# Performance work log

Measured on AMD Instinct MI355X. Metric: run time of the kernel, lower is better.

Reference implementation:

```python
import jax, jax.numpy as jnp
import numpy as np

BETA = 0.35

def setup_inputs() -> dict:
    key = jax.random.key(0)
    k1, k2, k3 = jax.random.split(key, 3)
    B, D, C, O = 16384, 512, 4096, 128
    x = jax.random.normal(k1, (B, D), dtype=jnp.float32)
    centers = jax.random.normal(k2, (C, D), dtype=jnp.float32)
    W = jax.random.normal(k3, (C, O), dtype=jnp.float32) * (1.0 / np.sqrt(C))
    b = jnp.zeros((O,), dtype=jnp.float32)
    return {"x": x, "centers": centers, "W": W, "b": b}

def reference(x, centers, W, b):
    # Squared Euclidean distances via the GEMM identity ||a-b||^2 = ||a||^2 + ||b||^2 - 2 a.b
    # (same math as expand_dims/subtract/square/reduce_sum, avoids [B,C,D] intermediate)
    x_sq = jnp.sum(x * x, axis=1, keepdims=True)          # [B,1]
    c_sq = jnp.sum(centers * centers, axis=1)             # [C]
    cross = x @ centers.T                                  # [B,C]
    sq_dist = x_sq + c_sq[None, :] - 2.0 * cross           # [B,C]
    rbf = jnp.exp(-BETA * sq_dist)                         # [B,C]
    return rbf @ W + b                                      # [B,O]
```

## Files before the change

kernel.cpp:

```cpp
#include <hip/hip_runtime.h>
#include <hip/hip_bf16.h>

typedef short bf16x8 __attribute__((ext_vector_type(8)));
typedef float f32x4 __attribute__((ext_vector_type(4)));
typedef float f32x16 __attribute__((ext_vector_type(16)));
typedef long l64x2 __attribute__((ext_vector_type(2)));
typedef int i32x8 __attribute__((ext_vector_type(8)));
typedef unsigned short u16;
typedef unsigned char u8;

#define NB2 (-0.35f * 1.44269504088896340736f)
#define P2C (0.70f * 1.44269504088896340736f)
#define MFS(a,b,c) __builtin_amdgcn_mfma_scale_f32_32x32x64_f8f6f4( \
    a, b, c, 0, 0, 0, 0x7F7F7F7F, 0, 0x7F7F7F7F)
#define MFB(a,b,c) __builtin_amdgcn_mfma_f32_32x32x16_bf16(a, b, c, 0, 0, 0)

__device__ __forceinline__ u16 f2bf(float f) {
  union { float f; unsigned int u; } v; v.f = f;
  unsigned int x = v.u;
  return (u16)((x + 0x7FFFu + ((x >> 16) & 1u)) >> 16);
}

__device__ __forceinline__ unsigned cvtpk(float lo, float hi) {
  unsigned r;
  asm("v_cvt_pk_bf16_f32 %0, %1, %2" : "=v"(r) : "v"(lo), "v"(hi));
  return r;
}

__device__ __forceinline__ void pswap(unsigned &a, unsigned &b) {
  asm volatile("v_permlane32_swap_b32 %0, %1" : "+v"(a), "+v"(b));
}

__device__ __forceinline__ u8 f2e4m3(float f) {
  unsigned int u = __float_as_uint(f);
  u8 s = (u8)((u >> 24) & 0x80u);
  float a = fabsf(f);
  if (a >= 448.f) return s | 0x7E;
  if (a < 0.015625f) return s | (u8)(int)rintf(a * 512.f);
  unsigned int m = u & 0x7fffffffu;
  unsigned int r = m + 0x7FFFFu + ((m >> 20) & 1u);
  return s | (u8)((((r >> 23) - 120u) << 3) | ((r >> 20) & 7u));
}

__device__ __forceinline__ unsigned int pk4(float a, float b, float c, float d) {
#if __has_builtin(__builtin_amdgcn_cvt_pk_fp8_f32)
  int v = __builtin_amdgcn_cvt_pk_fp8_f32(a, b, 0, false);
  v = __builtin_amdgcn_cvt_pk_fp8_f32(c, d, v, true);
  return (unsigned int)v;
#else
  return (unsigned int)f2e4m3(a) | ((unsigned int)f2e4m3(b) << 8)
       | ((unsigned int)f2e4m3(c) << 16) | ((unsigned int)f2e4m3(d) << 24);
#endif
}

#define GLOAD_LDS(g, l) __builtin_amdgcn_global_load_lds( \
    (const __attribute__((address_space(1))) unsigned int*)(g), \
    (__attribute__((address_space(3))) unsigned int*)(l), 16, 0, 0)

__global__ __launch_bounds__(512)
void prep_x8(const float* __restrict__ src, u8* __restrict__ dst,
             float* __restrict__ sq) {
  const int row = blockIdx.x * 8 + (threadIdx.x >> 6);
  const int i6 = threadIdx.x & 63;
  const float4* p = (const float4*)(src + (size_t)row * 512) + i6 * 2;
  float4 a = p[0], b = p[1];
  float ss = a.x*a.x + a.y*a.y + a.z*a.z + a.w*a.w
           + b.x*b.x + b.y*b.y + b.z*b.z + b.w*b.w;
  uint2 o;
  o.x = pk4(a.x, a.y, a.z, a.w);
  o.y = pk4(b.x, b.y, b.z, b.w);
  const int P = i6 >> 3, rem = i6 & 7;
  const int kh = rem >> 2;
  const int l = (kh << 5) | (row & 31);
  *(uint2*)(dst + (size_t)(row >> 5) * 16384 + P * 2048 + l * 32 + (rem & 3) * 8) = o;
  ss += __shfl_xor(ss, 1);  ss += __shfl_xor(ss, 2);
  ss += __shfl_xor(ss, 4);  ss += __shfl_xor(ss, 8);
  ss += __shfl_xor(ss, 16); ss += __shfl_xor(ss, 32);
  if (i6 == 0) sq[row] = ss;
}

__global__ __launch_bounds__(256)
void prep_cen(const float* __restrict__ cen, u8* __restrict__ cfr,
              float* __restrict__ csq) {
  const int t = threadIdx.x;
  const int c = blockIdx.x * 4 + (t >> 6);
  const int i6 = t & 63;
  const float* p = cen + (size_t)c * 512 + i6 * 8;
  float4 a = *(const float4*)p, b = *(const float4*)(p + 4);
  float ss = a.x*a.x + a.y*a.y + a.z*a.z + a.w*a.w
           + b.x*b.x + b.y*b.y + b.z*b.z + b.w*b.w;
  uint2 o;
  o.x = pk4(a.x, a.y, a.z, a.w);
  o.y = pk4(b.x, b.y, b.z, b.w);
  const int P = i6 >> 3, rem = i6 & 7;
  const int kh = rem >> 2;
  const int lc = c & 31;
  const int l = (kh << 5) | lc;
  const int u = (rem >> 1) & 1;
  const int sub = rem & 1;
  const int us = u ^ ((lc >> 2) & 1);
  *(uint2*)(cfr + (size_t)(c >> 5) * 16384 + P * 2048 + l * 32 + us * 16 + sub * 8) = o;
  ss += __shfl_xor(ss, 1);  ss += __shfl_xor(ss, 2);
  ss += __shfl_xor(ss, 4);  ss += __shfl_xor(ss, 8);
  ss += __shfl_xor(ss, 16); ss += __shfl_xor(ss, 32);
  if (i6 == 0) csq[c] = ss;
}

__global__ __launch_bounds__(256)
void prep_w(const float* __restrict__ W, u8* __restrict__ wt) {
  __shared__ u16 t_[128 * 66];
  const int c0 = blockIdx.x * 64;
  const int t = threadIdx.x;
#pragma unroll
  for (int it = 0; it < 32; ++it) {
    int idx = it * 256 + t;
    int cl = idx >> 7;
    int o  = idx & 127;
    t_[o * 66 + cl] = f2bf(W[(size_t)(c0 + cl) * 128 + o]);
  }
  __syncthreads();
#pragma unroll
  for (int it = 0; it < 4; ++it) {
    int idx = it * 256 + t;
    int o  = idx >> 3;
    int uu = idx & 7;
    int ch = uu >> 2;
    int kt = (uu >> 1) & 1;
    int h2 = uu & 1;
    int u  = (kt * 2 + h2) ^ ((o >> 1) & 3);
    u16* d = (u16*)(wt + ((size_t)(c0 >> 5) + ch) * 8192 + o * 64 + u * 16);
    const u16* s_ = &t_[o * 66 + ch * 32 + kt * 16 + h2 * 8];
#pragma unroll
    for (int j = 0; j < 8; ++j) d[j] = s_[j];
  }
}

__global__ __launch_bounds__(256)
void init_out(const float* __restrict__ bias, float* __restrict__ out) {
  const int i4 = blockIdx.x * 256 + threadIdx.x;
  float4 b = ((const float4*)bias)[i4 & 31];
  ((float4*)out)[i4] = b;
}

__global__ __launch_bounds__(256, 2)
void rbf_main(const u8* __restrict__ xfs, const u8* __restrict__ cfr,
              const u8* __restrict__ wtgb, const float* __restrict__ csq_g,
              const float* __restrict__ xsq_g, float* __restrict__ out)
{
  __shared__ __align__(16) u8 cs[2][16384];
  __shared__ __align__(16) u8 wt[2][8192];
  __shared__ __align__(16) float csq_l[1024];
  __shared__ __align__(16) float xsq_l[128];

  const int tid = threadIdx.x;
  const int lane = tid & 63;
  const int wv = tid >> 6;
  const int l31 = lane & 31;
  const int h = lane >> 5;
  const int bid = blockIdx.x;
  const int chq = bid & 3;
  const size_t r0 = (size_t)(bid >> 2) * 128;

#define S_CS(cc) do { \
    const u8* sG_ = cfr + ((size_t)(chq * 32 + (cc)) << 14) + tid * 16; \
    u8* sL_ = &cs[(cc) & 1][0] + tid * 16; \
    GLOAD_LDS(sG_,         sL_); \
    GLOAD_LDS(sG_ + 4096,  sL_ + 4096); \
    GLOAD_LDS(sG_ + 8192,  sL_ + 8192); \
    GLOAD_LDS(sG_ + 12288, sL_ + 12288); \
  } while (0)

#define S_W(cc) do { \
    const u8* wg_ = wtgb + ((size_t)(chq * 32 + (cc)) << 13) + tid * 16; \
    u8* wl_ = &wt[(cc) & 1][0] + tid * 16; \
    GLOAD_LDS(wg_,        wl_); \
    GLOAD_LDS(wg_ + 4096, wl_ + 4096); \
  } while (0)

  if (tid < 32) GLOAD_LDS(xsq_g + r0 + tid * 4, xsq_l + tid * 4);
  GLOAD_LDS(csq_g + chq * 1024 + tid * 4, csq_l + tid * 4);
  S_CS(0);
  S_W(0);

  i32x8 xf8[8];
  {
    const u8* xb = xfs + ((size_t)((bid >> 2) * 4 + wv)) * 16384 + lane * 32;
#pragma unroll
    for (int P = 0; P < 8; ++P) {
      union { l64x2 q[2]; i32x8 v; } t;
      t.q[0] = *(const l64x2*)(xb + P * 2048);
      t.q[1] = *(const l64x2*)(xb + P * 2048 + 16);
      xf8[P] = t.v;
    }
  }

  asm volatile("s_waitcnt vmcnt(0)" ::: "memory");
  __builtin_amdgcn_s_barrier();
  __builtin_amdgcn_sched_barrier(0);

  const float xn = NB2 * xsq_l[wv * 32 + l31];

  const int swz = (lane >> 2) & 1;
  const int alo = lane * 32 + swz * 16;
  const int ahi = lane * 32 + (swz ^ 1) * 16;
  const int wsw = (l31 >> 1) & 3;
  const int wb_o = l31 * 64;
  const int wu0 = ((0 + h) ^ wsw) << 4;
  const int wu1 = ((2 + h) ^ wsw) << 4;

  const f32x16 z16 = {0,0,0,0,0,0,0,0,0,0,0,0,0,0,0,0};
  f32x16 oa0 = z16, oa1 = z16, oa2 = z16, oa3 = z16;

#pragma unroll 1
  for (int cc = 0; cc < 32; ++cc) {
    if (cc < 31) { S_CS(cc + 1); S_W(cc + 1); }
    const u8* csb = &cs[cc & 1][0];

    f32x16 s0 = z16, s1 = z16;
#pragma unroll
    for (int P = 0; P < 8; ++P) {
      union { l64x2 q[2]; i32x8 v; } A;
      A.q[0] = *(const l64x2*)(csb + P * 2048 + alo);
      A.q[1] = *(const l64x2*)(csb + P * 2048 + ahi);
      __builtin_amdgcn_s_setprio(1);
      if (P & 1) s1 = MFS(A.v, xf8[P], s1);
      else       s0 = MFS(A.v, xf8[P], s0);
      __builtin_amdgcn_s_setprio(0);
    }

    f32x4 cq0 = *(const f32x4*)(csq_l + cc * 32 + 0  + 4 * h);
    f32x4 cq1 = *(const f32x4*)(csq_l + cc * 32 + 8  + 4 * h);
    f32x4 cq2 = *(const f32x4*)(csq_l + cc * 32 + 16 + 4 * h);
    f32x4 cq3 = *(const f32x4*)(csq_l + cc * 32 + 24 + 4 * h);
    float e[16];
#pragma unroll
    for (int r = 0; r < 16; ++r) {
      const float cq = (r < 4 ? cq0[r] : r < 8 ? cq1[r - 4] : r < 12 ? cq2[r - 8] : cq3[r - 12]);
      e[r] = __builtin_amdgcn_exp2f(fmaf(s0[r] + s1[r], P2C, fmaf(cq, NB2, xn)));
    }
    unsigned P0 = cvtpk(e[0],  e[1]),  P1 = cvtpk(e[2],  e[3]);
    unsigned P2 = cvtpk(e[4],  e[5]),  P3 = cvtpk(e[6],  e[7]);
    unsigned P4 = cvtpk(e[8],  e[9]),  P5 = cvtpk(e[10], e[11]);
    unsigned P6 = cvtpk(e[12], e[13]), P7 = cvtpk(e[14], e[15]);
    pswap(P0, P2); pswap(P1, P3);
    pswap(P4, P6); pswap(P5, P7);
    union { unsigned u[4]; bf16x8 v; } FA, GA;
    FA.u[0] = P0; FA.u[1] = P1; FA.u[2] = P2; FA.u[3] = P3;
    GA.u[0] = P4; GA.u[1] = P5; GA.u[2] = P6; GA.u[3] = P7;

    {
      const u8* wtb = &wt[cc & 1][0];
      bf16x8 wA0 = *(const bf16x8*)(wtb + wb_o + wu0);
      bf16x8 wB0 = *(const bf16x8*)(wtb + wb_o + wu1);
      bf16x8 wA1 = *(const bf16x8*)(wtb + 2048 + wb_o + wu0);
      bf16x8 wB1 = *(const bf16x8*)(wtb + 2048 + wb_o + wu1);
      __builtin_amdgcn_s_setprio(1);
      oa0 = MFB(FA.v, wA0, oa0);
      oa0 = MFB(GA.v, wB0, oa0);
      oa1 = MFB(FA.v, wA1, oa1);
      oa1 = MFB(GA.v, wB1, oa1);
      __builtin_amdgcn_s_setprio(0);
      bf16x8 wA2 = *(const bf16x8*)(wtb + 4096 + wb_o + wu0);
      bf16x8 wB2 = *(const bf16x8*)(wtb + 4096 + wb_o + wu1);
      bf16x8 wA3 = *(const bf16x8*)(wtb + 6144 + wb_o + wu0);
      bf16x8 wB3 = *(const bf16x8*)(wtb + 6144 + wb_o + wu1);
      __builtin_amdgcn_s_setprio(1);
      oa2 = MFB(FA.v, wA2, oa2);
      oa2 = MFB(GA.v, wB2, oa2);
      oa3 = MFB(FA.v, wA3, oa3);
      oa3 = MFB(GA.v, wB3, oa3);
      __builtin_amdgcn_s_setprio(0);
    }

    asm volatile("s_waitcnt vmcnt(0)" ::: "memory");
    __builtin_amdgcn_s_barrier();
    __builtin_amdgcn_sched_barrier(0);
  }

#pragma unroll
  for (int r = 0; r < 16; ++r) {
    const int m = wv * 32 + (r & 3) + 8 * (r >> 2) + 4 * h;
    float* op = &out[(r0 + m) * 128 + l31];
    atomicAdd(op,      oa0[r]);
    atomicAdd(op + 32, oa1[r]);
    atomicAdd(op + 64, oa2[r]);
    atomicAdd(op + 96, oa3[r]);
  }
#undef S_CS
#undef S_W
}

extern "C" void kernel_launch(void* const* d_in, const int* in_sizes, int n_in,
                              void* d_out, int out_size, void* d_ws, size_t ws_size,
                              hipStream_t stream) {
  (void)in_sizes; (void)n_in; (void)out_size; (void)ws_size;
  const float* x   = (const float*)d_in[0];
  const float* cen = (const float*)d_in[1];
  const float* W   = (const float*)d_in[2];
  const float* b   = (const float*)d_in[3];
  u8* xfs = (u8*)d_ws;
  u8* cfr = xfs + (size_t)16384 * 512;
  u8* wtgb = cfr + (size_t)4096 * 512;
  float* csq = (float*)(wtgb + (size_t)128 * 4096 * 2);
  float* xsq = csq + 4096;
  prep_x8<<<2048, 512, 0, stream>>>(x, xfs, xsq);
  prep_cen<<<1024, 256, 0, stream>>>(cen, cfr, csq);
  prep_w<<<64, 256, 0, stream>>>(W, wtgb);
  init_out<<<2048, 256, 0, stream>>>(b, (float*)d_out);
  rbf_main<<<512, 256, 0, stream>>>(xfs, cfr, wtgb, csq, xsq, (float*)d_out);
}
```

Measured before the change: 93.51 us.

## Switch second GEMM to FP8 scaled MFMA with W fragments read from global

Replaces the bf16 rbf@W stage with FP8 e4m3 scaled MFMA (32x32x64). W is pre-quantized with a 64x scale compensated by the MFMA scale exponent, and the rbf values are packed to fp8. Each iteration now processes two center chunks (K=64), and W fragments are loaded directly from global into registers instead of being staged in LDS. The center tile buffer grows to four slots so two chunks are prefetched per step. This halves the MFMA count and W bandwidth for the second GEMM and removes the W LDS traffic, at the cost of lower precision in the rbf and W operands.

```diff
diff --git a/kernel.cpp b/kernel.cpp
--- a/kernel.cpp
+++ b/kernel.cpp
@@ -1,7 +1,6 @@
 #include <hip/hip_runtime.h>
 #include <hip/hip_bf16.h>
 
-typedef short bf16x8 __attribute__((ext_vector_type(8)));
 typedef float f32x4 __attribute__((ext_vector_type(4)));
 typedef float f32x16 __attribute__((ext_vector_type(16)));
 typedef long l64x2 __attribute__((ext_vector_type(2)));
@@ -13,19 +12,8 @@
 #define P2C (0.70f * 1.44269504088896340736f)
 #define MFS(a,b,c) __builtin_amdgcn_mfma_scale_f32_32x32x64_f8f6f4( \
     a, b, c, 0, 0, 0, 0x7F7F7F7F, 0, 0x7F7F7F7F)
-#define MFB(a,b,c) __builtin_amdgcn_mfma_f32_32x32x16_bf16(a, b, c, 0, 0, 0)
-
-__device__ __forceinline__ u16 f2bf(float f) {
-  union { float f; unsigned int u; } v; v.f = f;
-  unsigned int x = v.u;
-  return (u16)((x + 0x7FFFu + ((x >> 16) & 1u)) >> 16);
-}
-
-__device__ __forceinline__ unsigned cvtpk(float lo, float hi) {
-  unsigned r;
-  asm("v_cvt_pk_bf16_f32 %0, %1, %2" : "=v"(r) : "v"(lo), "v"(hi));
-  return r;
-}
+#define MFS2(a,b,c) __builtin_amdgcn_mfma_scale_f32_32x32x64_f8f6f4( \
+    a, b, c, 0, 0, 0, 0x7F7F7F7F, 0, 0x79797979)
 
 __device__ __forceinline__ void pswap(unsigned &a, unsigned &b) {
   asm volatile("v_permlane32_swap_b32 %0, %1" : "+v"(a), "+v"(b));
@@ -107,32 +95,25 @@
 }
 
 __global__ __launch_bounds__(256)
-void prep_w(const float* __restrict__ W, u8* __restrict__ wt) {
-  __shared__ u16 t_[128 * 66];
-  const int c0 = blockIdx.x * 64;
+void prep_w(const float* __restrict__ W, u8* __restrict__ wfr) {
+  __shared__ float t_[64 * 128];
+  const int pr = blockIdx.x;
   const int t = threadIdx.x;
 #pragma unroll
   for (int it = 0; it < 32; ++it) {
     int idx = it * 256 + t;
-    int cl = idx >> 7;
-    int o  = idx & 127;
-    t_[o * 66 + cl] = f2bf(W[(size_t)(c0 + cl) * 128 + o]);
+    t_[idx] = W[(size_t)(pr * 64 + (idx >> 7)) * 128 + (idx & 127)];
   }
   __syncthreads();
-#pragma unroll
-  for (int it = 0; it < 4; ++it) {
-    int idx = it * 256 + t;
-    int o  = idx >> 3;
-    int uu = idx & 7;
-    int ch = uu >> 2;
-    int kt = (uu >> 1) & 1;
-    int h2 = uu & 1;
-    int u  = (kt * 2 + h2) ^ ((o >> 1) & 3);
-    u16* d = (u16*)(wt + ((size_t)(c0 >> 5) + ch) * 8192 + o * 64 + u * 16);
-    const u16* s_ = &t_[o * 66 + ch * 32 + kt * 16 + h2 * 8];
-#pragma unroll
-    for (int j = 0; j < 8; ++j) d[j] = s_[j];
-  }
+  const int l = t & 63, ot = t >> 6;
+  const int kh = l >> 5, o = ot * 32 + (l & 31);
+  u8 buf[32];
+#pragma unroll
+  for (int b = 0; b < 32; ++b)
+    buf[b] = f2e4m3(64.f * t_[(kh * 32 + b) * 128 + o]);
+  u8* d = wfr + (size_t)pr * 8192 + ot * 2048 + l * 32;
+  *(uint4*)d = *(uint4*)buf;
+  *(uint4*)(d + 16) = *(uint4*)(buf + 16);
 }
 
 __global__ __launch_bounds__(256)
@@ -144,11 +125,10 @@
 
 __global__ __launch_bounds__(256, 2)
 void rbf_main(const u8* __restrict__ xfs, const u8* __restrict__ cfr,
-              const u8* __restrict__ wtgb, const float* __restrict__ csq_g,
+              const u8* __restrict__ wfr, const float* __restrict__ csq_g,
               const float* __restrict__ xsq_g, float* __restrict__ out)
 {
-  __shared__ __align__(16) u8 cs[2][16384];
-  __shared__ __align__(16) u8 wt[2][8192];
+  __shared__ __align__(16) u8 cs[4][16384];
   __shared__ __align__(16) float csq_l[1024];
   __shared__ __align__(16) float xsq_l[128];
 
@@ -163,24 +143,17 @@
 
 #define S_CS(cc) do { \
     const u8* sG_ = cfr + ((size_t)(chq * 32 + (cc)) << 14) + tid * 16; \
-    u8* sL_ = &cs[(cc) & 1][0] + tid * 16; \
+    u8* sL_ = &cs[(cc) & 3][0] + tid * 16; \
     GLOAD_LDS(sG_,         sL_); \
     GLOAD_LDS(sG_ + 4096,  sL_ + 4096); \
     GLOAD_LDS(sG_ + 8192,  sL_ + 8192); \
     GLOAD_LDS(sG_ + 12288, sL_ + 12288); \
   } while (0)
 
-#define S_W(cc) do { \
-    const u8* wg_ = wtgb + ((size_t)(chq * 32 + (cc)) << 13) + tid * 16; \
-    u8* wl_ = &wt[(cc) & 1][0] + tid * 16; \
-    GLOAD_LDS(wg_,        wl_); \
-    GLOAD_LDS(wg_ + 4096, wl_ + 4096); \
-  } while (0)
-
   if (tid < 32) GLOAD_LDS(xsq_g + r0 + tid * 4, xsq_l + tid * 4);
   GLOAD_LDS(csq_g + chq * 1024 + tid * 4, csq_l + tid * 4);
   S_CS(0);
-  S_W(0);
+  S_CS(1);
 
   i32x8 xf8[8];
   {
@@ -203,74 +176,66 @@
   const int swz = (lane >> 2) & 1;
   const int alo = lane * 32 + swz * 16;
   const int ahi = lane * 32 + (swz ^ 1) * 16;
-  const int wsw = (l31 >> 1) & 3;
-  const int wb_o = l31 * 64;
-  const int wu0 = ((0 + h) ^ wsw) << 4;
-  const int wu1 = ((2 + h) ^ wsw) << 4;
 
   const f32x16 z16 = {0,0,0,0,0,0,0,0,0,0,0,0,0,0,0,0};
   f32x16 oa0 = z16, oa1 = z16, oa2 = z16, oa3 = z16;
 
+#define G1EXP(CC, SLOT, O0, O1, O2, O3) do { \
+    const u8* csb = &cs[SLOT][0]; \
+    f32x16 s0 = z16, s1 = z16; \
+    _Pragma("unroll") \
+    for (int P = 0; P < 8; ++P) { \
+      union { l64x2 q[2]; i32x8 v; } A; \
+      A.q[0] = *(const l64x2*)(csb + P * 2048 + alo); \
+      A.q[1] = *(const l64x2*)(csb + P * 2048 + ahi); \
+      __builtin_amdgcn_s_setprio(1); \
+      if (P & 1) s1 = MFS(A.v, xf8[P], s1); \
+      else       s0 = MFS(A.v, xf8[P], s0); \
+      __builtin_amdgcn_s_setprio(0); \
+    } \
+    f32x4 cq0 = *(const f32x4*)(csq_l + (CC) * 32 + 0  + 4 * h); \
+    f32x4 cq1 = *(const f32x4*)(csq_l + (CC) * 32 + 8  + 4 * h); \
+    f32x4 cq2 = *(const f32x4*)(csq_l + (CC) * 32 + 16 + 4 * h); \
+    f32x4 cq3 = *(const f32x4*)(csq_l + (CC) * 32 + 24 + 4 * h); \
+    float e[16]; \
+    _Pragma("unroll") \
+    for (int r = 0; r < 16; ++r) { \
+      const float cq = (r < 4 ? cq0[r] : r < 8 ? cq1[r-4] : r < 12 ? cq2[r-8] : cq3[r-12]); \
+      e[r] = __builtin_amdgcn_exp2f(fmaf(s0[r] + s1[r], P2C, fmaf(cq, NB2, xn))); \
+    } \
+    O0 = pk4(e[0],  e[1],  e[2],  e[3]); \
+    O1 = pk4(e[4],  e[5],  e[6],  e[7]); \
+    O2 = pk4(e[8],  e[9],  e[10], e[11]); \
+    O3 = pk4(e[12], e[13], e[14], e[15]); \
+  } while (0)
+
 #pragma unroll 1
-  for (int cc = 0; cc < 32; ++cc) {
-    if (cc < 31) { S_CS(cc + 1); S_W(cc + 1); }
-    const u8* csb = &cs[cc & 1][0];
-
-    f32x16 s0 = z16, s1 = z16;
-#pragma unroll
-    for (int P = 0; P < 8; ++P) {
-      union { l64x2 q[2]; i32x8 v; } A;
-      A.q[0] = *(const l64x2*)(csb + P * 2048 + alo);
-      A.q[1] = *(const l64x2*)(csb + P * 2048 + ahi);
-      __builtin_amdgcn_s_setprio(1);
-      if (P & 1) s1 = MFS(A.v, xf8[P], s1);
-      else       s0 = MFS(A.v, xf8[P], s0);
-      __builtin_amdgcn_s_setprio(0);
-    }
-
-    f32x4 cq0 = *(const f32x4*)(csq_l + cc * 32 + 0  + 4 * h);
-    f32x4 cq1 = *(const f32x4*)(csq_l + cc * 32 + 8  + 4 * h);
-    f32x4 cq2 = *(const f32x4*)(csq_l + cc * 32 + 16 + 4 * h);
-    f32x4 cq3 = *(const f32x4*)(csq_l + cc * 32 + 24 + 4 * h);
-    float e[16];
-#pragma unroll
-    for (int r = 0; r < 16; ++r) {
-      const float cq = (r < 4 ? cq0[r] : r < 8 ? cq1[r - 4] : r < 12 ? cq2[r - 8] : cq3[r - 12]);
-      e[r] = __builtin_amdgcn_exp2f(fmaf(s0[r] + s1[r], P2C, fmaf(cq, NB2, xn)));
-    }
-    unsigned P0 = cvtpk(e[0],  e[1]),  P1 = cvtpk(e[2],  e[3]);
-    unsigned P2 = cvtpk(e[4],  e[5]),  P3 = cvtpk(e[6],  e[7]);
-    unsigned P4 = cvtpk(e[8],  e[9]),  P5 = cvtpk(e[10], e[11]);
-    unsigned P6 = cvtpk(e[12], e[13]), P7 = cvtpk(e[14], e[15]);
-    pswap(P0, P2); pswap(P1, P3);
-    pswap(P4, P6); pswap(P5, P7);
-    union { unsigned u[4]; bf16x8 v; } FA, GA;
-    FA.u[0] = P0; FA.u[1] = P1; FA.u[2] = P2; FA.u[3] = P3;
-    GA.u[0] = P4; GA.u[1] = P5; GA.u[2] = P6; GA.u[3] = P7;
-
-    {
-      const u8* wtb = &wt[cc & 1][0];
-      bf16x8 wA0 = *(const bf16x8*)(wtb + wb_o + wu0);
-      bf16x8 wB0 = *(const bf16x8*)(wtb + wb_o + wu1);
-      bf16x8 wA1 = *(const bf16x8*)(wtb + 2048 + wb_o + wu0);
-      bf16x8 wB1 = *(const bf16x8*)(wtb + 2048 + wb_o + wu1);
-      __builtin_amdgcn_s_setprio(1);
-      oa0 = MFB(FA.v, wA0, oa0);
-      oa0 = MFB(GA.v, wB0, oa0);
-      oa1 = MFB(FA.v, wA1, oa1);
-      oa1 = MFB(GA.v, wB1, oa1);
-      __builtin_amdgcn_s_setprio(0);
-      bf16x8 wA2 = *(const bf16x8*)(wtb + 4096 + wb_o + wu0);
-      bf16x8 wB2 = *(const bf16x8*)(wtb + 4096 + wb_o + wu1);
-      bf16x8 wA3 = *(const bf16x8*)(wtb + 6144 + wb_o + wu0);
-      bf16x8 wB3 = *(const bf16x8*)(wtb + 6144 + wb_o + wu1);
-      __builtin_amdgcn_s_setprio(1);
-      oa2 = MFB(FA.v, wA2, oa2);
-      oa2 = MFB(GA.v, wB2, oa2);
-      oa3 = MFB(FA.v, wA3, oa3);
-      oa3 = MFB(GA.v, wB3, oa3);
-      __builtin_amdgcn_s_setprio(0);
-    }
+  for (int t = 0; t < 16; ++t) {
+    const u8* wgb = wfr + ((size_t)(chq * 16 + t) << 13) + lane * 32;
+    union { l64x2 q[2]; i32x8 v; } w0, w1, w2, w3;
+    w0.q[0] = *(const l64x2*)(wgb);        w0.q[1] = *(const l64x2*)(wgb + 16);
+    w1.q[0] = *(const l64x2*)(wgb + 2048); w1.q[1] = *(const l64x2*)(wgb + 2064);
+    w2.q[0] = *(const l64x2*)(wgb + 4096); w2.q[1] = *(const l64x2*)(wgb + 4112);
+    w3.q[0] = *(const l64x2*)(wgb + 6144); w3.q[1] = *(const l64x2*)(wgb + 6160);
+    __builtin_amdgcn_sched_barrier(0);
+    if (t < 15) { S_CS(2 * t + 2); S_CS(2 * t + 3); }
+    __builtin_amdgcn_sched_barrier(0);
+
+    unsigned D0, D1, D2, D3, E0, E1, E2, E3;
+    G1EXP(2 * t,     (2 * t) & 3,     D0, D1, D2, D3);
+    G1EXP(2 * t + 1, (2 * t + 1) & 3, E0, E1, E2, E3);
+
+    pswap(D0, E0); pswap(D1, E1); pswap(D2, E2); pswap(D3, E3);
+    union { unsigned u[8]; i32x8 v; } PA;
+    PA.u[0] = D0; PA.u[1] = E0; PA.u[2] = D1; PA.u[3] = E1;
+    PA.u[4] = D2; PA.u[5] = E2; PA.u[6] = D3; PA.u[7] = E3;
+
+    __builtin_amdgcn_s_setprio(1);
+    oa0 = MFS2(PA.v, w0.v, oa0);
+    oa1 = MFS2(PA.v, w1.v, oa1);
+    oa2 = MFS2(PA.v, w2.v, oa2);
+    oa3 = MFS2(PA.v, w3.v, oa3);
+    __builtin_amdgcn_s_setprio(0);
 
     asm volatile("s_waitcnt vmcnt(0)" ::: "memory");
     __builtin_amdgcn_s_barrier();
@@ -287,7 +252,7 @@
     atomicAdd(op + 96, oa3[r]);
   }
 #undef S_CS
-#undef S_W
+#undef G1EXP
 }
 
 extern "C" void kernel_launch(void* const* d_in, const int* in_sizes, int n_in,
@@ -300,12 +265,12 @@
   const float* b   = (const float*)d_in[3];
   u8* xfs = (u8*)d_ws;
   u8* cfr = xfs + (size_t)16384 * 512;
-  u8* wtgb = cfr + (size_t)4096 * 512;
-  float* csq = (float*)(wtgb + (size_t)128 * 4096 * 2);
+  u8* wfr = cfr + (size_t)4096 * 512;
+  float* csq = (float*)(wfr + (size_t)64 * 8192);
   float* xsq = csq + 4096;
   prep_x8<<<2048, 512, 0, stream>>>(x, xfs, xsq);
   prep_cen<<<1024, 256, 0, stream>>>(cen, cfr, csq);
-  prep_w<<<64, 256, 0, stream>>>(W, wtgb);
+  prep_w<<<64, 256, 0, stream>>>(W, wfr);
   init_out<<<2048, 256, 0, stream>>>(b, (float*)d_out);
-  rbf_main<<<512, 256, 0, stream>>>(xfs, cfr, wtgb, csq, xsq, (float*)d_out);
-}
+  rbf_main<<<512, 256, 0, stream>>>(xfs, cfr, wfr, csq, xsq, (float*)d_out);
+}
```

Result: faster. 87.93 us, median of 2 (-6.0%).
